# Kernel optimization log

Measured on AMD Instinct MI355X. Metric: run time of the kernel, lower is better.

## Reference

```python
import jax, jax.numpy as jnp
import numpy as np

DMODEL = 1024
DK = 64
DHEAD = 16
DEPTH = DK * DHEAD
N, LQ, L = 2, 2048, 2048


def setup_inputs() -> dict:
    key = jax.random.key(0)
    ks = jax.random.split(key, 12)
    s = 1.0 / np.sqrt(DMODEL)
    inp = {
        'x': jax.random.normal(ks[0], (N, LQ, DMODEL), jnp.float32),
        'y': jax.random.normal(ks[1], (N, L, DMODEL), jnp.float32),
        'mask': jnp.tril(jnp.ones((LQ, L), dtype=bool)),  # causal
        'Wq': jax.random.normal(ks[2], (DMODEL, DEPTH), jnp.float32) * s,
        'bq': jnp.zeros((DEPTH,), jnp.float32),
        'Wk': jax.random.normal(ks[3], (DMODEL, DEPTH), jnp.float32) * s,
        'bk': jnp.zeros((DEPTH,), jnp.float32),
        'Wv': jax.random.normal(ks[4], (DMODEL, DEPTH), jnp.float32) * s,
        'bv': jnp.zeros((DEPTH,), jnp.float32),
        'Wo': jax.random.normal(ks[5], (DEPTH, DMODEL), jnp.float32) * (1.0 / np.sqrt(DEPTH)),
        'bo': jnp.zeros((DMODEL,), jnp.float32),
    }
    return inp


def reference(x, y, mask, Wq, bq, Wk, bk, Wv, bv, Wo, bo):
    fac = 1.0 / np.sqrt(DK)
    q = (x @ Wq + bq).reshape(N, LQ, DHEAD, DK).transpose(0, 2, 1, 3)  # N,H,Lq,dk
    k = (y @ Wk + bk).reshape(N, L, DHEAD, DK).transpose(0, 2, 1, 3)   # N,H,L,dk
    v = (y @ Wv + bv).reshape(N, L, DHEAD, DK).transpose(0, 2, 1, 3)   # N,H,L,dk
    scores = jnp.einsum('bhqd,bhkd->bhqk', q, k) * fac                 # N,H,Lq,L
    scores = jnp.where(mask, scores, -1e9)  # mask broadcasts over N,H
    attn = jax.nn.softmax(scores, axis=-1)
    out = jnp.einsum('bhqk,bhkd->bhqd', attn, v)                        # N,H,Lq,dk
    out = out.transpose(0, 2, 1, 3).reshape(N, LQ, DEPTH)
    return out @ Wo + bo
```

## Files before the change

kernel.cpp:

```cpp
#include <hip/hip_runtime.h>
#include <hip/hip_bf16.h>

typedef __attribute__((ext_vector_type(8))) short short8;
typedef __attribute__((ext_vector_type(4))) float floatx4;

#define LQ 2048
#define DM 1024
#define NH 16
#define LOG2E 1.44269504088896f

typedef __attribute__((address_space(1))) void gas_t;
typedef __attribute__((address_space(3))) void las_t;

__device__ __forceinline__ void async16(const __hip_bfloat16* g, __hip_bfloat16* l) {
    __builtin_amdgcn_global_load_lds((gas_t*)g, (las_t*)l, 16, 0, 0);
}

__global__ __launch_bounds__(256) void prep_all(
    const float* __restrict__ x,  const float* __restrict__ y,
    const float* __restrict__ Wq, const float* __restrict__ Wk,
    const float* __restrict__ Wv, const float* __restrict__ Wo,
    __hip_bfloat16* __restrict__ xb,  __hip_bfloat16* __restrict__ yb,
    __hip_bfloat16* __restrict__ Wqt, __hip_bfloat16* __restrict__ Wkt,
    __hip_bfloat16* __restrict__ Wvt, __hip_bfloat16* __restrict__ Wot)
{
    __shared__ float tile[64][65];
    const int t  = threadIdx.x;
    const int bx = blockIdx.x;

    if (bx < 4096) {
        const float* in = (bx < 2048) ? x : y;
        __hip_bfloat16* out = (bx < 2048) ? xb : yb;
        const int i = ((bx & 2047) * 256 + t) * 8;
        float4 a0 = ((const float4*)(in + i))[0];
        float4 a1 = ((const float4*)(in + i))[1];
        union { __hip_bfloat16 h[8]; uint4 u; } pk;
        pk.h[0] = __float2bfloat16(a0.x); pk.h[1] = __float2bfloat16(a0.y);
        pk.h[2] = __float2bfloat16(a0.z); pk.h[3] = __float2bfloat16(a0.w);
        pk.h[4] = __float2bfloat16(a1.x); pk.h[5] = __float2bfloat16(a1.y);
        pk.h[6] = __float2bfloat16(a1.z); pk.h[7] = __float2bfloat16(a1.w);
        *(uint4*)(out + i) = pk.u;
        return;
    }

    const int r    = bx - 4096;
    const int wsel = r >> 8;
    const int tid  = r & 255;
    const int n0   = (tid & 15) * 64, k0 = (tid >> 4) * 64;
    const float* W = (wsel == 0) ? Wq : (wsel == 1) ? Wk : (wsel == 2) ? Wv : Wo;
    __hip_bfloat16* Wt = (wsel == 0) ? Wqt : (wsel == 1) ? Wkt : (wsel == 2) ? Wvt : Wot;

    const int rr0 = t >> 4, c4 = (t & 15) * 4;
#pragma unroll
    for (int rr = 0; rr < 64; rr += 16) {
        float4 v = *(const float4*)&W[(size_t)(k0 + rr0 + rr) * DM + n0 + c4];
        tile[rr0 + rr][c4 + 0] = v.x; tile[rr0 + rr][c4 + 1] = v.y;
        tile[rr0 + rr][c4 + 2] = v.z; tile[rr0 + rr][c4 + 3] = v.w;
    }
    __syncthreads();
    const int nr = t >> 2, kc = (t & 3) * 16;
    union { __hip_bfloat16 h[16]; uint4 u[2]; } pk;
#pragma unroll
    for (int i = 0; i < 16; ++i) pk.h[i] = __float2bfloat16(tile[kc + i][nr]);
    uint4* dst = (uint4*)&Wt[(size_t)(n0 + nr) * DM + k0 + kc];
    dst[0] = pk.u[0];
    dst[1] = pk.u[1];
}

__global__ __launch_bounds__(256) void gemm_qkv(
    const __hip_bfloat16* __restrict__ xb,
    const __hip_bfloat16* __restrict__ yb,
    const __hip_bfloat16* __restrict__ Bt,
    const float* __restrict__ bq, const float* __restrict__ bk,
    const float* __restrict__ bv,
    __hip_bfloat16* __restrict__ Qb, __hip_bfloat16* __restrict__ Kb,
    __hip_bfloat16* __restrict__ Vt,
    float qscl)
{
    constexpr int BM = 128, BN = 128, BK = 32, Kd = 1024;
    __shared__ __align__(16) __hip_bfloat16 As[2][BM * BK];
    __shared__ __align__(16) __hip_bfloat16 Bs[2][BN * BK];

    const int t    = threadIdx.x;
    const int w    = t >> 6;
    const int lane = t & 63;
    const int quad = lane >> 4;
    const int l16  = lane & 15;
    const int wm   = w & 1;
    const int wn   = w >> 1;
    const int m0   = blockIdx.y * BM;
    const int n0   = blockIdx.x * BN;
    const int region = n0 >> 10;
    const int nl     = n0 & 1023;

    const __hip_bfloat16* A = (region == 0) ? xb : yb;

    const int lrow = lane >> 2;
    const int lcol = (lane & 3) * 8;

    floatx4 acc[4][4];
#pragma unroll
    for (int i = 0; i < 4; ++i)
#pragma unroll
        for (int j = 0; j < 4; ++j) acc[i][j] = (floatx4){0.f, 0.f, 0.f, 0.f};

    auto stage = [&](int k0, int buf) {
#pragma unroll
        for (int s = 0; s < 2; ++s) {
            const int seg = w * 2 + s;
            async16(A + (size_t)(m0 + seg * 16 + lrow) * Kd + k0 + lcol,
                    &As[buf][seg * 16 * BK]);
            async16(Bt + (size_t)(n0 + seg * 16 + lrow) * Kd + k0 + lcol,
                    &Bs[buf][seg * 16 * BK]);
        }
    };

    stage(0, 0);
    int cur = 0;
    for (int k0 = 0; k0 < Kd; k0 += BK) {
        __syncthreads();
        if (k0 + BK < Kd) stage(k0 + BK, cur ^ 1);

        short8 af[4], bf[4];
#pragma unroll
        for (int i = 0; i < 4; ++i)
            af[i] = *(const short8*)&As[cur][(wm * 64 + i * 16 + l16) * BK + quad * 8];
#pragma unroll
        for (int j = 0; j < 4; ++j)
            bf[j] = *(const short8*)&Bs[cur][(wn * 64 + j * 16 + l16) * BK + quad * 8];
#pragma unroll
        for (int i = 0; i < 4; ++i)
#pragma unroll
            for (int j = 0; j < 4; ++j)
                acc[i][j] = __builtin_amdgcn_mfma_f32_16x16x32_bf16(af[i], bf[j], acc[i][j], 0, 0, 0);
        cur ^= 1;
    }

    if (region < 2) {
        __hip_bfloat16* C    = (region == 0) ? Qb : Kb;
        const float*    bias = (region == 0) ? bq : bk;
        const float     scl  = (region == 0) ? qscl : 1.0f;
#pragma unroll
        for (int j = 0; j < 4; ++j) {
            const int col = nl + wn * 64 + j * 16 + l16;
            const float bvv = bias[col];
#pragma unroll
            for (int i = 0; i < 4; ++i) {
#pragma unroll
                for (int r = 0; r < 4; ++r) {
                    const int row = m0 + wm * 64 + i * 16 + quad * 4 + r;
                    C[(size_t)row * 1024 + col] = __float2bfloat16((acc[i][j][r] + bvv) * scl);
                }
            }
        }
    } else {
#pragma unroll
        for (int j = 0; j < 4; ++j) {
            const int col = nl + wn * 64 + j * 16 + l16;
            const float bvv = bv[col];
#pragma unroll
            for (int i = 0; i < 4; ++i) {
                const int row0 = m0 + wm * 64 + i * 16 + quad * 4;
                union { __hip_bfloat16 h4[4]; uint2 u; } pk;
#pragma unroll
                for (int r = 0; r < 4; ++r)
                    pk.h4[r] = __float2bfloat16(acc[i][j][r] + bvv);
                *(uint2*)&Vt[((size_t)((row0 >> 11) * 1024 + col)) * 2048 + (row0 & 2047)] = pk.u;
            }
        }
    }
}

template <int MODE>
__global__ __launch_bounds__(256) void gemm128(
    const __hip_bfloat16* __restrict__ A,
    const __hip_bfloat16* __restrict__ Bt,
    const float* __restrict__ bias0,
    const float* __restrict__ bias1,
    void* __restrict__ C0v, void* __restrict__ C1v,
    int M, int N, int K, float scale)
{
    constexpr int BM = 128, BN = 128, BK = 32;
    __shared__ __align__(16) __hip_bfloat16 As[2][BM * BK];
    __shared__ __align__(16) __hip_bfloat16 Bs[2][BN * BK];

    const int t    = threadIdx.x;
    const int w    = t >> 6;
    const int lane = t & 63;
    const int quad = lane >> 4;
    const int l16  = lane & 15;
    const int wm   = w & 1;
    const int wn   = w >> 1;
    const int m0   = blockIdx.y * BM;
    const int n0   = blockIdx.x * BN;

    const int lrow = lane >> 2;
    const int lcol = (lane & 3) * 8;

    floatx4 acc[4][4];
#pragma unroll
    for (int i = 0; i < 4; ++i)
#pragma unroll
        for (int j = 0; j < 4; ++j) acc[i][j] = (floatx4){0.f, 0.f, 0.f, 0.f};

    auto stage = [&](int k0, int buf) {
#pragma unroll
        for (int s = 0; s < 2; ++s) {
            const int seg = w * 2 + s;
            async16(A + (size_t)(m0 + seg * 16 + lrow) * K + k0 + lcol,
                    &As[buf][seg * 16 * BK]);
            async16(Bt + (size_t)(n0 + seg * 16 + lrow) * K + k0 + lcol,
                    &Bs[buf][seg * 16 * BK]);
        }
    };

    stage(0, 0);
    int cur = 0;
    for (int k0 = 0; k0 < K; k0 += BK) {
        __syncthreads();
        if (k0 + BK < K) stage(k0 + BK, cur ^ 1);

        short8 af[4], bf[4];
#pragma unroll
        for (int i = 0; i < 4; ++i)
            af[i] = *(const short8*)&As[cur][(wm * 64 + i * 16 + l16) * BK + quad * 8];
#pragma unroll
        for (int j = 0; j < 4; ++j)
            bf[j] = *(const short8*)&Bs[cur][(wn * 64 + j * 16 + l16) * BK + quad * 8];
#pragma unroll
        for (int i = 0; i < 4; ++i)
#pragma unroll
            for (int j = 0; j < 4; ++j)
                acc[i][j] = __builtin_amdgcn_mfma_f32_16x16x32_bf16(af[i], bf[j], acc[i][j], 0, 0, 0);
        cur ^= 1;
    }

    const bool second = (MODE == 2) && (n0 >= 1024);
    const float* bias = second ? bias1 : bias0;
    void* Cv          = second ? C1v : C0v;
    const int  nbase  = n0 - (second ? 1024 : 0);
    const int  Nout   = (MODE == 2) ? 1024 : N;

#pragma unroll
    for (int j = 0; j < 4; ++j) {
        const int col = nbase + wn * 64 + j * 16 + l16;
        const float bv = bias[col];
#pragma unroll
        for (int i = 0; i < 4; ++i) {
#pragma unroll
            for (int r = 0; r < 4; ++r) {
                const int row = m0 + wm * 64 + i * 16 + quad * 4 + r;
                const float v = (acc[i][j][r] + bv) * scale;
                if constexpr (MODE == 1) ((float*)Cv)[(size_t)row * Nout + col] = v;
                else ((__hip_bfloat16*)Cv)[(size_t)row * Nout + col] = __float2bfloat16(v);
            }
        }
    }
}

template <bool A_IS_F32, bool OUT_F32, bool TRANSV = false>
__global__ __launch_bounds__(256) void gemm64(
    const void* __restrict__ Av,
    const float* __restrict__ B,
    const float* __restrict__ bias,
    void* __restrict__ Cv,
    int M, int N, int K, float scale)
{
    __shared__ __align__(16) __hip_bfloat16 As[64][40];
    __shared__ __align__(16) __hip_bfloat16 Bs[64][40];

    const int t    = threadIdx.x;
    const int wave = t >> 6;
    const int lane = t & 63;
    const int quad = lane >> 4;
    const int l16  = lane & 15;
    const int m0   = blockIdx.y * 64;
    const int n0   = blockIdx.x * 64;

    floatx4 acc[4];
#pragma unroll
    for (int i = 0; i < 4; ++i) acc[i] = (floatx4){0.f, 0.f, 0.f, 0.f};

    const int arow = t >> 2, acol = (t & 3) * 8;
    const int bkk  = t >> 3, bnn  = (t & 7) * 8;

    for (int k0 = 0; k0 < K; k0 += 32) {
        if constexpr (A_IS_F32) {
            const float* A = (const float*)Av;
            const float* ap = A + (size_t)(m0 + arow) * K + k0 + acol;
            float4 a0 = ((const float4*)ap)[0];
            float4 a1 = ((const float4*)ap)[1];
            union { __hip_bfloat16 h[8]; short8 s; } up;
            up.h[0] = __float2bfloat16(a0.x); up.h[1] = __float2bfloat16(a0.y);
            up.h[2] = __float2bfloat16(a0.z); up.h[3] = __float2bfloat16(a0.w);
            up.h[4] = __float2bfloat16(a1.x); up.h[5] = __float2bfloat16(a1.y);
            up.h[6] = __float2bfloat16(a1.z); up.h[7] = __float2bfloat16(a1.w);
            *(short8*)(&As[arow][acol]) = up.s;
        } else {
            const __hip_bfloat16* A = (const __hip_bfloat16*)Av;
            uint4 av = *(const uint4*)(A + (size_t)(m0 + arow) * K + k0 + acol);
            *(uint4*)(&As[arow][acol]) = av;
        }
        {
            const float* bp = B + (size_t)(k0 + bkk) * N + n0 + bnn;
            float4 b0 = ((const float4*)bp)[0];
            float4 b1 = ((const float4*)bp)[1];
            Bs[bnn + 0][bkk] = __float2bfloat16(b0.x);
            Bs[bnn + 1][bkk] = __float2bfloat16(b0.y);
            Bs[bnn + 2][bkk] = __float2bfloat16(b0.z);
            Bs[bnn + 3][bkk] = __float2bfloat16(b0.w);
            Bs[bnn + 4][bkk] = __float2bfloat16(b1.x);
            Bs[bnn + 5][bkk] = __float2bfloat16(b1.y);
            Bs[bnn + 6][bkk] = __float2bfloat16(b1.z);
            Bs[bnn + 7][bkk] = __float2bfloat16(b1.w);
        }
        __syncthreads();

        short8 afrag = *(const short8*)(&As[wave * 16 + l16][quad * 8]);
#pragma unroll
        for (int nt = 0; nt < 4; ++nt) {
            short8 bfrag = *(const short8*)(&Bs[nt * 16 + l16][quad * 8]);
            acc[nt] = __builtin_amdgcn_mfma_f32_16x16x32_bf16(afrag, bfrag, acc[nt], 0, 0, 0);
        }
        __syncthreads();
    }

#pragma unroll
    for (int nt = 0; nt < 4; ++nt) {
        const int col = n0 + nt * 16 + l16;
        const float bvf = bias[col];
        if constexpr (TRANSV) {
            const int row0 = m0 + wave * 16 + quad * 4;
            union { __hip_bfloat16 h4[4]; uint2 u; } pk;
#pragma unroll
            for (int r = 0; r < 4; ++r)
                pk.h4[r] = __float2bfloat16(acc[nt][r] + bvf);
            *(uint2*)&((__hip_bfloat16*)Cv)[((size_t)((row0 >> 11) * 1024 + col)) * 2048 + (row0 & 2047)] = pk.u;
        } else {
#pragma unroll
            for (int r = 0; r < 4; ++r) {
                const int row = m0 + wave * 16 + quad * 4 + r;
                const float v = (acc[nt][r] + bvf) * scale;
                if constexpr (OUT_F32) ((float*)Cv)[(size_t)row * N + col] = v;
                else ((__hip_bfloat16*)Cv)[(size_t)row * N + col] = __float2bfloat16(v);
            }
        }
    }
}

#define PP 72

__global__ __launch_bounds__(256, 3) void attn_mfma6(
    const __hip_bfloat16* __restrict__ Q,
    const __hip_bfloat16* __restrict__ K,
    const __hip_bfloat16* __restrict__ Vt,
    __hip_bfloat16* __restrict__ O)
{
    __shared__ __align__(16) __hip_bfloat16 KtS[2][64 * 64];
    __shared__ __align__(16) __hip_bfloat16 VtS[2][64 * 64];
    __shared__ __align__(16) __hip_bfloat16 PsQ[128 * PP];

    const int t    = threadIdx.x;
    const int w    = t >> 6;
    const int lane = t & 63;
    const int quad = lane >> 4;
    const int l16  = lane & 15;
    const int b    = blockIdx.z;
    const int h    = blockIdx.y;
    const int qx   = gridDim.x - 1 - blockIdx.x;
    const int q0   = qx * 128;

    const size_t rowbase = (size_t)b * LQ;
    const int    hcol    = h * 64;
    const size_t vbase   = (size_t)(b * NH + h) * 64 * LQ;

    const int r8 = l16 & 7;

    auto stage = [&](int j0n, int buf) {
#pragma unroll
        for (int rnd = 0; rnd < 2; ++rnd) {
            const int c   = rnd * 256 + t;
            const int row = c >> 3;
            const int ch  = (c & 7) ^ (row & 7);
            async16(K + (rowbase + j0n + row) * DM + hcol + ch * 8,
                    &KtS[buf][c * 8]);
            async16(Vt + vbase + (size_t)row * LQ + j0n + ch * 8,
                    &VtS[buf][c * 8]);
        }
    };

    {
        const int qrow = t >> 1, qseg = (t & 1) * 32;
        const uint4* src = (const uint4*)(Q + (rowbase + q0 + qrow) * DM + hcol + qseg);
        uint4* dst = (uint4*)&PsQ[qrow * PP + qseg];
        dst[0] = src[0]; dst[1] = src[1]; dst[2] = src[2]; dst[3] = src[3];
    }
    stage(0, 0);
    __syncthreads();

    short8 qf[2][2];
#pragma unroll
    for (int g = 0; g < 2; ++g)
#pragma unroll
        for (int hh = 0; hh < 2; ++hh)
            qf[g][hh] = *(const short8*)&PsQ[(w * 32 + g * 16 + l16) * PP + hh * 32 + quad * 8];

    __hip_bfloat16* Pw = &PsQ[(w * 32) * PP];

    float l_i[2] = {0.f, 0.f};
    floatx4 o[2][4];
#pragma unroll
    for (int g = 0; g < 2; ++g)
#pragma unroll
        for (int i = 0; i < 4; ++i) o[g][i] = (floatx4){0.f, 0.f, 0.f, 0.f};

    const int wq_lo  = q0 + w * 32;
    const int wq_hi  = wq_lo + 31;
    const int ntiles = 2 * qx + 2;

    for (int jt = 0; jt < ntiles; ++jt) {
        const int j0  = jt * 64;
        const int cur = jt & 1;

        __syncthreads();
        if (jt + 1 < ntiles) stage(j0 + 64, cur ^ 1);

        if (j0 <= wq_hi) {
            const bool bnd = (j0 + 63 > wq_lo);
#pragma unroll
            for (int jc = 0; jc < 4; ++jc) {
                const __hip_bfloat16* kr = &KtS[cur][(jc * 16 + l16) * 64];
                short8 ak0 = *(const short8*)&kr[((quad    ) ^ r8) * 8];
                short8 ak1 = *(const short8*)&kr[((quad + 4) ^ r8) * 8];
#pragma unroll
                for (int g = 0; g < 2; ++g) {
                    floatx4 z = (floatx4){0.f, 0.f, 0.f, 0.f};
                    z = __builtin_amdgcn_mfma_f32_16x16x32_bf16(ak0, qf[g][0], z, 0, 0, 0);
                    z = __builtin_amdgcn_mfma_f32_16x16x32_bf16(ak1, qf[g][1], z, 0, 0, 0);
                    if (bnd) {
                        const int qg = wq_lo + g * 16 + l16;
#pragma unroll
                        for (int r = 0; r < 4; ++r) {
                            const int j = j0 + jc * 16 + quad * 4 + r;
                            if (j > qg) z[r] = -1e30f;
                        }
                    }
                    union { __hip_bfloat16 h4[4]; uint2 u; } pk;
#pragma unroll
                    for (int r = 0; r < 4; ++r) {
                        const float e = __builtin_amdgcn_exp2f(z[r]);
                        l_i[g] += e;
                        pk.h4[r] = __float2bfloat16(e);
                    }
                    *(uint2*)&Pw[(g * 16 + l16) * PP + jc * 16 + quad * 4] = pk.u;
                }
            }
            short8 pa[2][2];
#pragma unroll
            for (int g = 0; g < 2; ++g) {
                pa[g][0] = *(const short8*)&Pw[(g * 16 + l16) * PP + quad * 8];
                pa[g][1] = *(const short8*)&Pw[(g * 16 + l16) * PP + 32 + quad * 8];
            }
#pragma unroll
            for (int subf = 0; subf < 4; ++subf) {
                const __hip_bfloat16* vr = &VtS[cur][(subf * 16 + l16) * 64];
                short8 vb0 = *(const short8*)&vr[((quad    ) ^ r8) * 8];
                short8 vb1 = *(const short8*)&vr[((quad + 4) ^ r8) * 8];
#pragma unroll
                for (int g = 0; g < 2; ++g) {
                    o[g][subf] = __builtin_amdgcn_mfma_f32_16x16x32_bf16(pa[g][0], vb0, o[g][subf], 0, 0, 0);
                    o[g][subf] = __builtin_amdgcn_mfma_f32_16x16x32_bf16(pa[g][1], vb1, o[g][subf], 0, 0, 0);
                }
            }
        }
    }

#pragma unroll
    for (int g = 0; g < 2; ++g) {
        l_i[g] += __shfl_xor(l_i[g], 16);
        l_i[g] += __shfl_xor(l_i[g], 32);
#pragma unroll
        for (int r = 0; r < 4; ++r) {
            const float linv = 1.0f / __shfl(l_i[g], quad * 4 + r);
            const size_t row = rowbase + q0 + w * 32 + g * 16 + quad * 4 + r;
#pragma unroll
            for (int subf = 0; subf < 4; ++subf)
                O[row * DM + hcol + subf * 16 + l16] = __float2bfloat16(o[g][subf][r] * linv);
        }
    }
}

extern "C" void kernel_launch(void* const* d_in, const int* in_sizes, int n_in,
                              void* d_out, int out_size, void* d_ws, size_t ws_size,
                              hipStream_t stream)
{
    (void)in_sizes; (void)n_in; (void)out_size;

    const float* x  = (const float*)d_in[0];
    const float* y  = (const float*)d_in[1];
    const float* Wq = (const float*)d_in[3];
    const float* bq = (const float*)d_in[4];
    const float* Wk = (const float*)d_in[5];
    const float* bk = (const float*)d_in[6];
    const float* Wv = (const float*)d_in[7];
    const float* bv = (const float*)d_in[8];
    const float* Wo = (const float*)d_in[9];
    const float* bo = (const float*)d_in[10];

    const size_t NTOK = (size_t)2 * LQ * DM;
    const size_t MM   = (size_t)DM * DM;
    const int    M    = 2 * LQ;
    const float  QSCL = 0.125f * LOG2E;

    __hip_bfloat16* Qb  = (__hip_bfloat16*)d_ws;
    __hip_bfloat16* Kb  = Qb + NTOK;
    __hip_bfloat16* Vtb = Kb + NTOK;
    __hip_bfloat16* Ab  = Vtb + NTOK;

    const size_t need = (4 * NTOK + 2 * NTOK + 4 * MM) * sizeof(__hip_bfloat16);
    const dim3 agrid(LQ / 128, NH, 2);

    if (ws_size >= need) {
        __hip_bfloat16* xb  = Ab + NTOK;
        __hip_bfloat16* yb  = xb + NTOK;
        __hip_bfloat16* Wqt = yb + NTOK;
        __hip_bfloat16* Wkt = Wqt + MM;
        __hip_bfloat16* Wvt = Wkt + MM;
        __hip_bfloat16* Wot = Wvt + MM;
        (void)Wkt; (void)Wvt;

        prep_all<<<5120, 256, 0, stream>>>(x, y, Wq, Wk, Wv, Wo,
                                           xb, yb, Wqt, Wkt, Wvt, Wot);

        const dim3 g3(3 * DM / 128, M / 128);
        const dim3 g1(DM / 128, M / 128);
        gemm_qkv<<<g3, 256, 0, stream>>>(xb, yb, Wqt, bq, bk, bv, Qb, Kb, Vtb, QSCL);
        attn_mfma6<<<agrid, 256, 0, stream>>>(Qb, Kb, Vtb, Ab);
        gemm128<1><<<g1, 256, 0, stream>>>(Ab, Wot, bo, bo, (float*)d_out, (float*)d_out, M, DM, DM, 1.0f);
    } else {
        const dim3 gblk(DM / 64, M / 64);
        gemm64<true,  false><<<gblk, 256, 0, stream>>>(x, Wq, bq, Qb, M, DM, DM, QSCL);
        gemm64<true,  false><<<gblk, 256, 0, stream>>>(y, Wk, bk, Kb, M, DM, DM, 1.0f);
        gemm64<true,  false, true><<<gblk, 256, 0, stream>>>(y, Wv, bv, Vtb, M, DM, DM, 1.0f);
        attn_mfma6<<<agrid, 256, 0, stream>>>(Qb, Kb, Vtb, Ab);
        gemm64<false, true ><<<gblk, 256, 0, stream>>>(Ab, Wo, bo, (float*)d_out, M, DM, DM, 1.0f);
    }
}
```

Before: 249.8 us.

## Load K and V fragments directly from global into registers in attention

```diff
diff --git a/kernel.cpp b/kernel.cpp
--- a/kernel.cpp
+++ b/kernel.cpp
@@ -350,15 +350,79 @@
 
 #define PP 72
 
-__global__ __launch_bounds__(256, 3) void attn_mfma6(
+#define LOADK(J0, DST)                                                        \
+    {                                                                         \
+        _Pragma("unroll")                                                     \
+        for (int jc = 0; jc < 4; ++jc) {                                      \
+            const __hip_bfloat16* kpp = kp + (size_t)((J0) + jc * 16) * DM;   \
+            DST[jc * 2]     = *(const short8*)(kpp);                          \
+            DST[jc * 2 + 1] = *(const short8*)(kpp + 32);                     \
+        }                                                                     \
+    }
+
+#define ATTN_TILE(JT, KARR)                                                   \
+    {                                                                         \
+        const int j0 = (JT) * 64;                                             \
+        short8 vb[8];                                                         \
+        _Pragma("unroll")                                                     \
+        for (int sf = 0; sf < 4; ++sf) {                                      \
+            const __hip_bfloat16* vpp = vp + (size_t)sf * 16 * LQ + j0;       \
+            vb[sf * 2]     = *(const short8*)(vpp);                           \
+            vb[sf * 2 + 1] = *(const short8*)(vpp + 32);                      \
+        }                                                                     \
+        const bool bnd = (j0 + 63 > wq_lo);                                   \
+        _Pragma("unroll")                                                     \
+        for (int jc = 0; jc < 4; ++jc) {                                      \
+            _Pragma("unroll")                                                 \
+            for (int g = 0; g < 2; ++g) {                                     \
+                floatx4 z = (floatx4){0.f, 0.f, 0.f, 0.f};                    \
+                z = __builtin_amdgcn_mfma_f32_16x16x32_bf16(KARR[jc * 2],     \
+                        qf[g][0], z, 0, 0, 0);                                \
+                z = __builtin_amdgcn_mfma_f32_16x16x32_bf16(KARR[jc * 2 + 1], \
+                        qf[g][1], z, 0, 0, 0);                                \
+                if (bnd) {                                                    \
+                    const int qg = wq_lo + g * 16 + l16;                      \
+                    _Pragma("unroll")                                         \
+                    for (int r = 0; r < 4; ++r) {                             \
+                        const int j = j0 + jc * 16 + quad * 4 + r;            \
+                        if (j > qg) z[r] = -1e30f;                            \
+                    }                                                         \
+                }                                                             \
+                union { __hip_bfloat16 h4[4]; uint2 u; } pk;                  \
+                _Pragma("unroll")                                             \
+                for (int r = 0; r < 4; ++r) {                                 \
+                    const float e = __builtin_amdgcn_exp2f(z[r]);             \
+                    lv[g][r] += e;                                            \
+                    pk.h4[r] = __float2bfloat16(e);                           \
+                }                                                             \
+                *(uint2*)&Pw[(g * 16 + l16) * PP + jc * 16 + quad * 4] = pk.u;\
+            }                                                                 \
+        }                                                                     \
+        short8 pa[2][2];                                                      \
+        _Pragma("unroll")                                                     \
+        for (int g = 0; g < 2; ++g) {                                         \
+            pa[g][0] = *(const short8*)&Pw[(g * 16 + l16) * PP + quad * 8];   \
+            pa[g][1] = *(const short8*)&Pw[(g * 16 + l16) * PP + 32 + quad * 8];\
+        }                                                                     \
+        _Pragma("unroll")                                                     \
+        for (int sf = 0; sf < 4; ++sf) {                                      \
+            _Pragma("unroll")                                                 \
+            for (int g = 0; g < 2; ++g) {                                     \
+                o[g][sf] = __builtin_amdgcn_mfma_f32_16x16x32_bf16(pa[g][0],  \
+                        vb[sf * 2], o[g][sf], 0, 0, 0);                       \
+                o[g][sf] = __builtin_amdgcn_mfma_f32_16x16x32_bf16(pa[g][1],  \
+                        vb[sf * 2 + 1], o[g][sf], 0, 0, 0);                   \
+            }                                                                 \
+        }                                                                     \
+    }
+
+__global__ __launch_bounds__(256, 2) void attn_mfma7(
     const __hip_bfloat16* __restrict__ Q,
     const __hip_bfloat16* __restrict__ K,
     const __hip_bfloat16* __restrict__ Vt,
     __hip_bfloat16* __restrict__ O)
 {
-    __shared__ __align__(16) __hip_bfloat16 KtS[2][64 * 64];
-    __shared__ __align__(16) __hip_bfloat16 VtS[2][64 * 64];
-    __shared__ __align__(16) __hip_bfloat16 PsQ[128 * PP];
+    __shared__ __align__(16) __hip_bfloat16 Ps[128 * PP];
 
     const int t    = threadIdx.x;
     const int w    = t >> 6;
@@ -374,118 +438,57 @@
     const int    hcol    = h * 64;
     const size_t vbase   = (size_t)(b * NH + h) * 64 * LQ;
 
-    const int r8 = l16 & 7;
-
-    auto stage = [&](int j0n, int buf) {
-#pragma unroll
-        for (int rnd = 0; rnd < 2; ++rnd) {
-            const int c   = rnd * 256 + t;
-            const int row = c >> 3;
-            const int ch  = (c & 7) ^ (row & 7);
-            async16(K + (rowbase + j0n + row) * DM + hcol + ch * 8,
-                    &KtS[buf][c * 8]);
-            async16(Vt + vbase + (size_t)row * LQ + j0n + ch * 8,
-                    &VtS[buf][c * 8]);
-        }
-    };
-
-    {
-        const int qrow = t >> 1, qseg = (t & 1) * 32;
-        const uint4* src = (const uint4*)(Q + (rowbase + q0 + qrow) * DM + hcol + qseg);
-        uint4* dst = (uint4*)&PsQ[qrow * PP + qseg];
-        dst[0] = src[0]; dst[1] = src[1]; dst[2] = src[2]; dst[3] = src[3];
-    }
-    stage(0, 0);
-    __syncthreads();
+    const int wq_lo = q0 + w * 32;
 
     short8 qf[2][2];
 #pragma unroll
     for (int g = 0; g < 2; ++g)
 #pragma unroll
         for (int hh = 0; hh < 2; ++hh)
-            qf[g][hh] = *(const short8*)&PsQ[(w * 32 + g * 16 + l16) * PP + hh * 32 + quad * 8];
-
-    __hip_bfloat16* Pw = &PsQ[(w * 32) * PP];
-
-    float l_i[2] = {0.f, 0.f};
+            qf[g][hh] = *(const short8*)(Q + (rowbase + wq_lo + g * 16 + l16) * DM
+                                         + hcol + hh * 32 + quad * 8);
+
+    __hip_bfloat16* Pw = &Ps[(w * 32) * PP];
+
+    floatx4 lv[2] = {(floatx4){0.f, 0.f, 0.f, 0.f}, (floatx4){0.f, 0.f, 0.f, 0.f}};
     floatx4 o[2][4];
 #pragma unroll
     for (int g = 0; g < 2; ++g)
 #pragma unroll
         for (int i = 0; i < 4; ++i) o[g][i] = (floatx4){0.f, 0.f, 0.f, 0.f};
 
-    const int wq_lo  = q0 + w * 32;
-    const int wq_hi  = wq_lo + 31;
-    const int ntiles = 2 * qx + 2;
-
-    for (int jt = 0; jt < ntiles; ++jt) {
-        const int j0  = jt * 64;
-        const int cur = jt & 1;
-
-        __syncthreads();
-        if (jt + 1 < ntiles) stage(j0 + 64, cur ^ 1);
-
-        if (j0 <= wq_hi) {
-            const bool bnd = (j0 + 63 > wq_lo);
-#pragma unroll
-            for (int jc = 0; jc < 4; ++jc) {
-                const __hip_bfloat16* kr = &KtS[cur][(jc * 16 + l16) * 64];
-                short8 ak0 = *(const short8*)&kr[((quad    ) ^ r8) * 8];
-                short8 ak1 = *(const short8*)&kr[((quad + 4) ^ r8) * 8];
-#pragma unroll
-                for (int g = 0; g < 2; ++g) {
-                    floatx4 z = (floatx4){0.f, 0.f, 0.f, 0.f};
-                    z = __builtin_amdgcn_mfma_f32_16x16x32_bf16(ak0, qf[g][0], z, 0, 0, 0);
-                    z = __builtin_amdgcn_mfma_f32_16x16x32_bf16(ak1, qf[g][1], z, 0, 0, 0);
-                    if (bnd) {
-                        const int qg = wq_lo + g * 16 + l16;
-#pragma unroll
-                        for (int r = 0; r < 4; ++r) {
-                            const int j = j0 + jc * 16 + quad * 4 + r;
-                            if (j > qg) z[r] = -1e30f;
-                        }
-                    }
-                    union { __hip_bfloat16 h4[4]; uint2 u; } pk;
-#pragma unroll
-                    for (int r = 0; r < 4; ++r) {
-                        const float e = __builtin_amdgcn_exp2f(z[r]);
-                        l_i[g] += e;
-                        pk.h4[r] = __float2bfloat16(e);
-                    }
-                    *(uint2*)&Pw[(g * 16 + l16) * PP + jc * 16 + quad * 4] = pk.u;
-                }
-            }
-            short8 pa[2][2];
-#pragma unroll
-            for (int g = 0; g < 2; ++g) {
-                pa[g][0] = *(const short8*)&Pw[(g * 16 + l16) * PP + quad * 8];
-                pa[g][1] = *(const short8*)&Pw[(g * 16 + l16) * PP + 32 + quad * 8];
-            }
-#pragma unroll
-            for (int subf = 0; subf < 4; ++subf) {
-                const __hip_bfloat16* vr = &VtS[cur][(subf * 16 + l16) * 64];
-                short8 vb0 = *(const short8*)&vr[((quad    ) ^ r8) * 8];
-                short8 vb1 = *(const short8*)&vr[((quad + 4) ^ r8) * 8];
-#pragma unroll
-                for (int g = 0; g < 2; ++g) {
-                    o[g][subf] = __builtin_amdgcn_mfma_f32_16x16x32_bf16(pa[g][0], vb0, o[g][subf], 0, 0, 0);
-                    o[g][subf] = __builtin_amdgcn_mfma_f32_16x16x32_bf16(pa[g][1], vb1, o[g][subf], 0, 0, 0);
-                }
-            }
-        }
+    const int my_nt = (wq_lo + 31) / 64 + 1;
+
+    const __hip_bfloat16* kp = K + (rowbase + l16) * DM + hcol + quad * 8;
+    const __hip_bfloat16* vp = Vt + vbase + (size_t)l16 * LQ + quad * 8;
+
+    short8 kaA[8], kaB[8];
+    LOADK(0, kaA);
+
+    int jt = 0;
+    while (true) {
+        if (jt + 1 < my_nt) LOADK((jt + 1) * 64, kaB);
+        ATTN_TILE(jt, kaA);
+        ++jt;
+        if (jt >= my_nt) break;
+        if (jt + 1 < my_nt) LOADK((jt + 1) * 64, kaA);
+        ATTN_TILE(jt, kaB);
+        ++jt;
+        if (jt >= my_nt) break;
     }
 
 #pragma unroll
     for (int g = 0; g < 2; ++g) {
-        l_i[g] += __shfl_xor(l_i[g], 16);
-        l_i[g] += __shfl_xor(l_i[g], 32);
+        float l_i = lv[g][0] + lv[g][1] + lv[g][2] + lv[g][3];
+        l_i += __shfl_xor(l_i, 16);
+        l_i += __shfl_xor(l_i, 32);
 #pragma unroll
         for (int r = 0; r < 4; ++r) {
-            const float linv = 1.0f / __shfl(l_i[g], quad * 4 + r);
+            const float linv = 1.0f / __shfl(l_i, quad * 4 + r);
             const size_t row = rowbase + q0 + w * 32 + g * 16 + quad * 4 + r;
 #pragma unroll
-            for (int subf = 0; subf < 4; ++subf)
-                O[row * DM + hcol + subf * 16 + l16] = __float2bfloat16(o[g][subf][r] * linv);
+            for (int sf = 0; sf < 4; ++sf)
+                O[row * DM + hcol + sf * 16 + l16] = __float2bfloat16(o[g][sf][r] * linv);
         }
     }
 }
@@ -535,14 +538,14 @@
         const dim3 g3(3 * DM / 128, M / 128);
         const dim3 g1(DM / 128, M / 128);
         gemm_qkv<<<g3, 256, 0, stream>>>(xb, yb, Wqt, bq, bk, bv, Qb, Kb, Vtb, QSCL);
-        attn_mfma6<<<agrid, 256, 0, stream>>>(Qb, Kb, Vtb, Ab);
+        attn_mfma7<<<agrid, 256, 0, stream>>>(Qb, Kb, Vtb, Ab);
         gemm128<1><<<g1, 256, 0, stream>>>(Ab, Wot, bo, bo, (float*)d_out, (float*)d_out, M, DM, DM, 1.0f);
     } else {
         const dim3 gblk(DM / 64, M / 64);
         gemm64<true,  false><<<gblk, 256, 0, stream>>>(x, Wq, bq, Qb, M, DM, DM, QSCL);
         gemm64<true,  false><<<gblk, 256, 0, stream>>>(y, Wk, bk, Kb, M, DM, DM, 1.0f);
         gemm64<true,  false, true><<<gblk, 256, 0, stream>>>(y, Wv, bv, Vtb, M, DM, DM, 1.0f);
-        attn_mfma6<<<agrid, 256, 0, stream>>>(Qb, Kb, Vtb, Ab);
+        attn_mfma7<<<agrid, 256, 0, stream>>>(Qb, Kb, Vtb, Ab);
         gemm64<false, true ><<<gblk, 256, 0, stream>>>(Ab, Wo, bo, (float*)d_out, M, DM, DM, 1.0f);
     }
 }
```

After: 306.5 us. 1.23x slower.

## Triple-buffer K/V tiles in attention with vmcnt waits and XCD-aware block mapping

Applied to the files above, without the earlier changes.

```diff
diff --git a/kernel.cpp b/kernel.cpp
--- a/kernel.cpp
+++ b/kernel.cpp
@@ -350,14 +350,14 @@
 
 #define PP 72
 
-__global__ __launch_bounds__(256, 3) void attn_mfma6(
+__global__ __launch_bounds__(256, 2) void attn_mfma8(
     const __hip_bfloat16* __restrict__ Q,
     const __hip_bfloat16* __restrict__ K,
     const __hip_bfloat16* __restrict__ Vt,
     __hip_bfloat16* __restrict__ O)
 {
-    __shared__ __align__(16) __hip_bfloat16 KtS[2][64 * 64];
-    __shared__ __align__(16) __hip_bfloat16 VtS[2][64 * 64];
+    __shared__ __align__(16) __hip_bfloat16 KtS[3][64 * 64];
+    __shared__ __align__(16) __hip_bfloat16 VtS[3][64 * 64];
     __shared__ __align__(16) __hip_bfloat16 PsQ[128 * PP];
 
     const int t    = threadIdx.x;
@@ -365,10 +365,13 @@
     const int lane = t & 63;
     const int quad = lane >> 4;
     const int l16  = lane & 15;
-    const int b    = blockIdx.z;
-    const int h    = blockIdx.y;
-    const int qx   = gridDim.x - 1 - blockIdx.x;
-    const int q0   = qx * 128;
+
+    const int f  = blockIdx.x;
+    const int p  = (f & 7) * 4 + ((f >> 3) >> 4);
+    const int qx = (f >> 3) & 15;
+    const int h  = p & 15;
+    const int b  = p >> 4;
+    const int q0 = qx * 128;
 
     const size_t rowbase = (size_t)b * LQ;
     const int    hcol    = h * 64;
@@ -396,7 +399,7 @@
         dst[0] = src[0]; dst[1] = src[1]; dst[2] = src[2]; dst[3] = src[3];
     }
     stage(0, 0);
-    __syncthreads();
+    stage(64, 1);
 
     short8 qf[2][2];
 #pragma unroll
@@ -418,12 +421,18 @@
     const int wq_hi  = wq_lo + 31;
     const int ntiles = 2 * qx + 2;
 
+    int cur = 0;
     for (int jt = 0; jt < ntiles; ++jt) {
-        const int j0  = jt * 64;
-        const int cur = jt & 1;
-
-        __syncthreads();
-        if (jt + 1 < ntiles) stage(j0 + 64, cur ^ 1);
+        const int j0 = jt * 64;
+
+        if (jt + 2 < ntiles) stage(j0 + 128, (cur + 2 >= 3) ? cur - 1 : cur + 2);
+
+        const int rem = (ntiles - 1 - jt > 2) ? 2 : (ntiles - 1 - jt);
+        if (rem >= 2)      asm volatile("s_waitcnt vmcnt(8)" ::: "memory");
+        else if (rem == 1) asm volatile("s_waitcnt vmcnt(4)" ::: "memory");
+        else               asm volatile("s_waitcnt vmcnt(0)" ::: "memory");
+        __builtin_amdgcn_sched_barrier(0);
+        __builtin_amdgcn_s_barrier();
 
         if (j0 <= wq_hi) {
             const bool bnd = (j0 + 63 > wq_lo);
@@ -473,6 +482,7 @@
                 }
             }
         }
+        cur = (cur + 1 >= 3) ? 0 : cur + 1;
     }
 
 #pragma unroll
@@ -518,7 +528,7 @@
     __hip_bfloat16* Ab  = Vtb + NTOK;
 
     const size_t need = (4 * NTOK + 2 * NTOK + 4 * MM) * sizeof(__hip_bfloat16);
-    const dim3 agrid(LQ / 128, NH, 2);
+    const dim3 agrid(512, 1, 1);
 
     if (ws_size >= need) {
         __hip_bfloat16* xb  = Ab + NTOK;
@@ -535,14 +545,14 @@
         const dim3 g3(3 * DM / 128, M / 128);
         const dim3 g1(DM / 128, M / 128);
         gemm_qkv<<<g3, 256, 0, stream>>>(xb, yb, Wqt, bq, bk, bv, Qb, Kb, Vtb, QSCL);
-        attn_mfma6<<<agrid, 256, 0, stream>>>(Qb, Kb, Vtb, Ab);
+        attn_mfma8<<<agrid, 256, 0, stream>>>(Qb, Kb, Vtb, Ab);
         gemm128<1><<<g1, 256, 0, stream>>>(Ab, Wot, bo, bo, (float*)d_out, (float*)d_out, M, DM, DM, 1.0f);
     } else {
         const dim3 gblk(DM / 64, M / 64);
         gemm64<true,  false><<<gblk, 256, 0, stream>>>(x, Wq, bq, Qb, M, DM, DM, QSCL);
         gemm64<true,  false><<<gblk, 256, 0, stream>>>(y, Wk, bk, Kb, M, DM, DM, 1.0f);
         gemm64<true,  false, true><<<gblk, 256, 0, stream>>>(y, Wv, bv, Vtb, M, DM, DM, 1.0f);
-        attn_mfma6<<<agrid, 256, 0, stream>>>(Qb, Kb, Vtb, Ab);
+        attn_mfma8<<<agrid, 256, 0, stream>>>(Qb, Kb, Vtb, Ab);
         gemm64<false, true ><<<gblk, 256, 0, stream>>>(Ab, Wo, bo, (float*)d_out, M, DM, DM, 1.0f);
     }
 }
```

Measured after the change: 242.4 us. 1.03x faster.
